# Performance work log

Hardware: AMD Instinct MI355X
Metric: run time of the kernel (lower is better)

## Reference

```python
import jax, jax.numpy as jnp
import numpy as np

D_MODEL = 1024
N_HEADS = 16
HEAD_DIM = D_MODEL // N_HEADS
ALPHA = 1.5
SEQ, BATCH = 4096, 8


def reduced_sparsemax(z, alpha):
    # projection of z/alpha onto the simplex along the last axis
    zs = z / alpha
    z_sorted = -jnp.sort(-zs, axis=-1)          # descending sort
    z_cumsum = jnp.cumsum(z_sorted, axis=-1)
    d = zs.shape[-1]
    r = jnp.arange(1, d + 1, dtype=zs.dtype)
    support = (z_sorted - (z_cumsum - 1.0) / r) > 0
    k = jnp.sum(support, axis=-1, keepdims=True)
    k_safe = jnp.clip(k, 1, None)
    tau_sum = jnp.take_along_axis(z_cumsum, k_safe - 1, axis=-1)
    tau = (tau_sum - 1.0) / k_safe.astype(zs.dtype)
    return jnp.clip(zs - tau, 0.0, None)


def setup_inputs() -> dict:
    key = jax.random.key(0)
    ks = jax.random.split(key, 11)
    s = 0.02
    return {
        "query": jax.random.normal(ks[0], (SEQ, BATCH, D_MODEL), jnp.float32),
        "key":   jax.random.normal(ks[1], (SEQ, BATCH, D_MODEL), jnp.float32),
        "value": jax.random.normal(ks[2], (SEQ, BATCH, D_MODEL), jnp.float32),
        "Wq": jax.random.normal(ks[3], (D_MODEL, D_MODEL), jnp.float32) * s,
        "bq": jnp.zeros((D_MODEL,), jnp.float32),
        "Wk": jax.random.normal(ks[4], (D_MODEL, D_MODEL), jnp.float32) * s,
        "bk": jnp.zeros((D_MODEL,), jnp.float32),
        "Wv": jax.random.normal(ks[5], (D_MODEL, D_MODEL), jnp.float32) * s,
        "bv": jnp.zeros((D_MODEL,), jnp.float32),
        "Wo": jax.random.normal(ks[6], (D_MODEL, D_MODEL), jnp.float32) * s,
        "bo": jnp.zeros((D_MODEL,), jnp.float32),
    }


def reference(query, key, value, Wq, bq, Wk, bk, Wv, bv, Wo, bo):
    A, B, D = query.shape  # (seq, batch, d_model) per the torch code's indexing
    H, hd = N_HEADS, HEAD_DIM
    Q = query @ Wq.T + bq
    K = key @ Wk.T + bk
    V = value @ Wv.T + bv
    # view(A, B, H, hd).transpose(0, 1) -> (B, A, H, hd)
    Q = jnp.swapaxes(Q.reshape(A, B, H, hd), 0, 1)
    K = jnp.swapaxes(K.reshape(A, B, H, hd), 0, 1)
    V = jnp.swapaxes(V.reshape(A, B, H, hd), 0, 1)
    # NOTE: faithful to the original code, attention is across HEADS:
    # scores shape (B, A, H, H)
    scores = jnp.einsum('bahd,bagd->bahg', Q, K) / jnp.sqrt(
        jnp.asarray(hd, jnp.float32))
    attn = reduced_sparsemax(scores, ALPHA)
    attn_out = jnp.einsum('bahg,bagd->bahd', attn, V)  # (B, A, H, hd)
    # transpose(1,2).view(B, -1, D): (B, H, A, hd) flattened to (B, A, D)
    attn_out = jnp.swapaxes(attn_out, 1, 2).reshape(B, -1, D)
    out = attn_out @ Wo.T + bo           # (B, A, D)
    return jnp.swapaxes(out, 0, 1)       # (A, B, D)
```

## Files before the change

### kernel.cpp

```cpp
#include <hip/hip_runtime.h>
#include <hip/hip_bf16.h>
#include <stdint.h>

typedef __bf16 bf16_t;
typedef __bf16 bf16x4 __attribute__((ext_vector_type(4)));
typedef __bf16 bf16x8 __attribute__((ext_vector_type(8)));
typedef float  f32x4  __attribute__((ext_vector_type(4)));

#define AS_G __attribute__((address_space(1)))
#define AS_L __attribute__((address_space(3)))

__global__ void cast_f32_bf16(const float* __restrict__ src, bf16_t* __restrict__ dst) {
    int i = blockIdx.x * 256 + threadIdx.x;
    float4 v = ((const float4*)src)[i];
    bf16x4 o;
    o.x = (bf16_t)v.x; o.y = (bf16_t)v.y; o.z = (bf16_t)v.z; o.w = (bf16_t)v.w;
    ((bf16x4*)dst)[i] = o;
}

template<int OUT_BF16>
__global__ void gemm_bt_kernel(const bf16_t* __restrict__ A,
                               const bf16_t* __restrict__ Bt,
                               const float* __restrict__ bias,
                               void* __restrict__ Cout,
                               int M, int N, int K) {
    __shared__ bf16_t As[128 * 32];
    __shared__ bf16_t Bs[128 * 32];
    const int tid  = threadIdx.x;
    const int wave = tid >> 6, lane = tid & 63;
    const int quad = lane >> 4, r16 = lane & 15;
    const int wm = (wave >> 1) * 64, wn = (wave & 1) * 64;
    const int m0 = blockIdx.y * 128, n0 = blockIdx.x * 128;

    const int sr = (wave << 5) + (lane >> 2);
    const int ce = (lane & 3) << 3;
    const bf16_t* ga = A  + (size_t)(m0 + sr) * K + ce;
    const bf16_t* gb = Bt + (size_t)(n0 + sr) * K + ce;
    bf16_t* la = &As[sr * 32 + ce];
    bf16_t* lb = &Bs[sr * 32 + ce];

    f32x4 acc[4][4] = {};

    for (int k0 = 0; k0 < K; k0 += 32) {
        __builtin_amdgcn_global_load_lds((AS_G void*)(ga + k0),              (AS_L void*)la,             16, 0, 0);
        __builtin_amdgcn_global_load_lds((AS_G void*)(ga + k0 + 16 * (size_t)K), (AS_L void*)(la + 16 * 32), 16, 0, 0);
        __builtin_amdgcn_global_load_lds((AS_G void*)(gb + k0),              (AS_L void*)lb,             16, 0, 0);
        __builtin_amdgcn_global_load_lds((AS_G void*)(gb + k0 + 16 * (size_t)K), (AS_L void*)(lb + 16 * 32), 16, 0, 0);
        __syncthreads();

        bf16x8 aF[4], bF[4];
#pragma unroll
        for (int t = 0; t < 4; ++t) {
            aF[t] = *(const bf16x8*)&As[(wm + t * 16 + r16) * 32 + quad * 8];
            bF[t] = *(const bf16x8*)&Bs[(wn + t * 16 + r16) * 32 + quad * 8];
        }
#pragma unroll
        for (int tm = 0; tm < 4; ++tm)
#pragma unroll
            for (int tn = 0; tn < 4; ++tn)
                acc[tm][tn] = __builtin_amdgcn_mfma_f32_16x16x32_bf16(aF[tm], bF[tn], acc[tm][tn], 0, 0, 0);
        __syncthreads();
    }

    float bv[4];
#pragma unroll
    for (int tn = 0; tn < 4; ++tn) bv[tn] = bias[n0 + wn + tn * 16 + r16];

#pragma unroll
    for (int tm = 0; tm < 4; ++tm) {
#pragma unroll
        for (int r = 0; r < 4; ++r) {
            const int m = m0 + wm + tm * 16 + quad * 4 + r;
#pragma unroll
            for (int tn = 0; tn < 4; ++tn) {
                const int n = n0 + wn + tn * 16 + r16;
                const float v = acc[tm][tn][r] + bv[tn];
                if (OUT_BF16) ((bf16_t*)Cout)[(size_t)m * N + n] = (bf16_t)v;
                else          ((float*)Cout)[(size_t)m * N + n]  = v;
            }
        }
    }
}

__global__ void attn_kernel(const bf16_t* __restrict__ Q, const bf16_t* __restrict__ K,
                            const bf16_t* __restrict__ V, bf16_t* __restrict__ M2) {
    __shared__ float zs_s[4][16][17];
    __shared__ float tau_s[4][16];
    const int wave = threadIdx.x >> 6, lane = threadIdx.x & 63;
    const int quad = lane >> 4, g16 = lane & 15;
    const int p = blockIdx.x * 4 + wave;
    const int a = p >> 3, b = p & 7;
    const bf16_t* q = Q + (size_t)p * 1024;
    const bf16_t* k = K + (size_t)p * 1024;
    const bf16_t* v = V + (size_t)p * 1024;

    bf16x8 qa0 = *(const bf16x8*)(q + g16 * 64 + quad * 8);
    bf16x8 qa1 = *(const bf16x8*)(q + g16 * 64 + 32 + quad * 8);
    bf16x8 ka0 = *(const bf16x8*)(k + g16 * 64 + quad * 8);
    bf16x8 ka1 = *(const bf16x8*)(k + g16 * 64 + 32 + quad * 8);
    f32x4 sc = {0.f, 0.f, 0.f, 0.f};
    sc = __builtin_amdgcn_mfma_f32_16x16x32_bf16(qa0, ka0, sc, 0, 0, 0);
    sc = __builtin_amdgcn_mfma_f32_16x16x32_bf16(qa1, ka1, sc, 0, 0, 0);

    const float inv = 1.0f / 12.0f;
#pragma unroll
    for (int r = 0; r < 4; ++r) zs_s[wave][quad * 4 + r][g16] = sc[r] * inv;
    __syncthreads();

    if (lane < 16) {
        float z[16];
#pragma unroll
        for (int j = 0; j < 16; ++j) z[j] = zs_s[wave][lane][j];
#pragma unroll
        for (int kk = 2; kk <= 16; kk <<= 1) {
#pragma unroll
            for (int j = kk >> 1; j > 0; j >>= 1) {
#pragma unroll
                for (int i = 0; i < 16; ++i) {
                    int ixj = i ^ j;
                    if (ixj > i) {
                        bool desc = ((i & kk) == 0);
                        float zi = z[i], zj = z[ixj];
                        bool sw = desc ? (zi < zj) : (zi > zj);
                        z[i]   = sw ? zj : zi;
                        z[ixj] = sw ? zi : zj;
                    }
                }
            }
        }
        float cum = 0.f, csel = 0.f;
        int ksel = 1;
#pragma unroll
        for (int j = 0; j < 16; ++j) {
            cum += z[j];
            bool sup = z[j] * (float)(j + 1) > (cum - 1.0f);
            ksel = sup ? (j + 1) : ksel;
            csel = sup ? cum : csel;
        }
        tau_s[wave][lane] = (csel - 1.0f) / (float)ksel;
    }
    __syncthreads();

#pragma unroll
    for (int r = 0; r < 4; ++r) {
        float av = sc[r] * inv - tau_s[wave][quad * 4 + r];
        zs_s[wave][quad * 4 + r][g16] = av > 0.f ? av : 0.f;
    }
    __syncthreads();

    bf16x8 aP;
#pragma unroll
    for (int j = 0; j < 8; ++j) {
        float f = (quad < 2) ? zs_s[wave][g16][quad * 8 + j] : 0.f;
        aP[j] = (bf16_t)f;
    }
#pragma unroll
    for (int c = 0; c < 4; ++c) {
        bf16x8 bV;
#pragma unroll
        for (int j = 0; j < 8; ++j) {
            int g = quad * 8 + j;
            bV[j] = (quad < 2) ? v[g * 64 + c * 16 + g16] : (bf16_t)0.f;
        }
        f32x4 oc = {0.f, 0.f, 0.f, 0.f};
        oc = __builtin_amdgcn_mfma_f32_16x16x32_bf16(aP, bV, oc, 0, 0, 0);
#pragma unroll
        for (int r = 0; r < 4; ++r) {
            int h = quad * 4 + r;
            int e = c * 16 + g16;
            int rr = (h << 8) + (a >> 4);
            int c2 = ((a & 15) << 6) + e;
            M2[((size_t)(rr * 8 + b)) * 1024 + c2] = (bf16_t)oc[r];
        }
    }
}

extern "C" void kernel_launch(void* const* d_in, const int* in_sizes, int n_in,
                              void* d_out, int out_size, void* d_ws, size_t ws_size,
                              hipStream_t stream) {
    (void)in_sizes; (void)n_in; (void)out_size; (void)ws_size;
    const float* query = (const float*)d_in[0];
    const float* key   = (const float*)d_in[1];
    const float* value = (const float*)d_in[2];
    const float* Wq = (const float*)d_in[3];
    const float* bq = (const float*)d_in[4];
    const float* Wk = (const float*)d_in[5];
    const float* bk = (const float*)d_in[6];
    const float* Wv = (const float*)d_in[7];
    const float* bv = (const float*)d_in[8];
    const float* Wo = (const float*)d_in[9];
    const float* bo = (const float*)d_in[10];

    const int M = 32768, D = 1024;
    const size_t MD = (size_t)M * D;

    uint8_t* ws = (uint8_t*)d_ws;
    bf16_t* abuf = (bf16_t*)ws;
    bf16_t* Qb   = (bf16_t*)(ws + MD * 2);
    bf16_t* Kb   = Qb + MD;
    bf16_t* Vb   = Kb + MD;
    bf16_t* M2   = Vb + MD;
    bf16_t* Wqb  = M2 + MD;
    bf16_t* Wkb  = Wqb + (size_t)D * D;
    bf16_t* Wvb  = Wkb + (size_t)D * D;
    bf16_t* Wob  = Wvb + (size_t)D * D;

    const int wBlocks = D * D / 1024;
    const int aBlocks = (int)(MD / 1024);
    cast_f32_bf16<<<wBlocks, 256, 0, stream>>>(Wq, Wqb);
    cast_f32_bf16<<<wBlocks, 256, 0, stream>>>(Wk, Wkb);
    cast_f32_bf16<<<wBlocks, 256, 0, stream>>>(Wv, Wvb);
    cast_f32_bf16<<<wBlocks, 256, 0, stream>>>(Wo, Wob);

    dim3 gg(D / 128, M / 128);

    cast_f32_bf16<<<aBlocks, 256, 0, stream>>>(query, abuf);
    gemm_bt_kernel<1><<<gg, 256, 0, stream>>>(abuf, Wqb, bq, Qb, M, D, D);
    cast_f32_bf16<<<aBlocks, 256, 0, stream>>>(key, abuf);
    gemm_bt_kernel<1><<<gg, 256, 0, stream>>>(abuf, Wkb, bk, Kb, M, D, D);
    cast_f32_bf16<<<aBlocks, 256, 0, stream>>>(value, abuf);
    gemm_bt_kernel<1><<<gg, 256, 0, stream>>>(abuf, Wvb, bv, Vb, M, D, D);

    attn_kernel<<<M / 4, 256, 0, stream>>>(Qb, Kb, Vb, M2);

    gemm_bt_kernel<0><<<gg, 256, 0, stream>>>(M2, Wob, bo, (float*)d_out, M, D, D);
}
```

Baseline: 875.2 us.

## Rework GEMM into 256x256 tiles with 4-stage LDS pipeline and swizzling

The GEMM kernel moves from 128x128 tiles with 4 waves to 256x256 tiles with 8 waves, using a 4-deep ring of LDS buffers. Global-to-LDS loads are issued three K-steps ahead and gated by vmcnt waits, which removes the per-step double barrier. LDS columns are XOR-swizzled to avoid bank conflicts, the block index is remapped for cache locality, and setprio raises priority during MFMA bursts. The aim is to hide memory latency and raise MFMA utilisation across all four projection GEMMs. The cost is 128KB of LDS per block and high register pressure from 32 accumulators per lane, which may limit occupancy.

```diff
diff --git a/kernel.cpp b/kernel.cpp
--- a/kernel.cpp
+++ b/kernel.cpp
@@ -19,61 +19,87 @@
 }
 
 template<int OUT_BF16>
-__global__ void gemm_bt_kernel(const bf16_t* __restrict__ A,
-                               const bf16_t* __restrict__ Bt,
-                               const float* __restrict__ bias,
-                               void* __restrict__ Cout,
-                               int M, int N, int K) {
-    __shared__ bf16_t As[128 * 32];
-    __shared__ bf16_t Bs[128 * 32];
+__global__ __launch_bounds__(512, 2)
+void gemm_bt_kernel(const bf16_t* __restrict__ A,
+                    const bf16_t* __restrict__ Bt,
+                    const float* __restrict__ bias,
+                    void* __restrict__ Cout,
+                    int M, int N, int K) {
+    __shared__ bf16_t smem[4][2][256 * 32];
+
     const int tid  = threadIdx.x;
     const int wave = tid >> 6, lane = tid & 63;
     const int quad = lane >> 4, r16 = lane & 15;
-    const int wm = (wave >> 1) * 64, wn = (wave & 1) * 64;
-    const int m0 = blockIdx.y * 128, n0 = blockIdx.x * 128;
-
-    const int sr = (wave << 5) + (lane >> 2);
-    const int ce = (lane & 3) << 3;
-    const bf16_t* ga = A  + (size_t)(m0 + sr) * K + ce;
-    const bf16_t* gb = Bt + (size_t)(n0 + sr) * K + ce;
-    bf16_t* la = &As[sr * 32 + ce];
-    bf16_t* lb = &Bs[sr * 32 + ce];
-
-    f32x4 acc[4][4] = {};
-
-    for (int k0 = 0; k0 < K; k0 += 32) {
-        __builtin_amdgcn_global_load_lds((AS_G void*)(ga + k0),              (AS_L void*)la,             16, 0, 0);
-        __builtin_amdgcn_global_load_lds((AS_G void*)(ga + k0 + 16 * (size_t)K), (AS_L void*)(la + 16 * 32), 16, 0, 0);
-        __builtin_amdgcn_global_load_lds((AS_G void*)(gb + k0),              (AS_L void*)lb,             16, 0, 0);
-        __builtin_amdgcn_global_load_lds((AS_G void*)(gb + k0 + 16 * (size_t)K), (AS_L void*)(lb + 16 * 32), 16, 0, 0);
-        __syncthreads();
-
-        bf16x8 aF[4], bF[4];
-#pragma unroll
-        for (int t = 0; t < 4; ++t) {
-            aF[t] = *(const bf16x8*)&As[(wm + t * 16 + r16) * 32 + quad * 8];
-            bF[t] = *(const bf16x8*)&Bs[(wn + t * 16 + r16) * 32 + quad * 8];
-        }
-#pragma unroll
-        for (int tm = 0; tm < 4; ++tm)
+    const int wr = wave >> 2, wc = wave & 3;
+
+    const int nbx = N >> 8;
+    const int cpx = gridDim.x >> 3;
+    const int swz = (blockIdx.x & 7) * cpx + (blockIdx.x >> 3);
+    const int m0 = (swz / nbx) << 8;
+    const int n0 = (swz % nbx) << 8;
+
+    const int c0 = tid, c1 = 512 + tid;
+    const int r0 = c0 >> 2, cc0 = c0 & 3;
+    const int r1 = c1 >> 2, cc1 = c1 & 3;
+    const int s0 = (r0 & 3) ^ ((r0 >> 2) & 3);
+    const int s1 = (r1 & 3) ^ ((r1 >> 2) & 3);
+    const bf16_t* gA0 = A  + (size_t)(m0 + r0) * K + ((cc0 ^ s0) << 3);
+    const bf16_t* gA1 = A  + (size_t)(m0 + r1) * K + ((cc1 ^ s1) << 3);
+    const bf16_t* gB0 = Bt + (size_t)(n0 + r0) * K + ((cc0 ^ s0) << 3);
+    const bf16_t* gB1 = Bt + (size_t)(n0 + r1) * K + ((cc1 ^ s1) << 3);
+
+#define STAGE(bufi, kt) do {                                                                    \
+        const int _ko = (kt) << 5;                                                              \
+        __builtin_amdgcn_global_load_lds((AS_G void*)(gA0 + _ko), (AS_L void*)(&smem[bufi][0][c0 * 8]), 16, 0, 0); \
+        __builtin_amdgcn_global_load_lds((AS_G void*)(gA1 + _ko), (AS_L void*)(&smem[bufi][0][c1 * 8]), 16, 0, 0); \
+        __builtin_amdgcn_global_load_lds((AS_G void*)(gB0 + _ko), (AS_L void*)(&smem[bufi][1][c0 * 8]), 16, 0, 0); \
+        __builtin_amdgcn_global_load_lds((AS_G void*)(gB1 + _ko), (AS_L void*)(&smem[bufi][1][c1 * 8]), 16, 0, 0); \
+    } while (0)
+
+    f32x4 acc[8][4] = {};
+    const int NT = K >> 5;
+
+    STAGE(0, 0); STAGE(1, 1); STAGE(2, 2);
+
+    const int swzc = quad ^ (r16 & 3) ^ ((r16 >> 2) & 3);
+    const int aoff = ((wr * 128 + r16) << 5) + (swzc << 3);
+    const int boff = ((wc * 64  + r16) << 5) + (swzc << 3);
+
+    for (int t = 0; t < NT; ++t) {
+        asm volatile("s_waitcnt vmcnt(8)\n\ts_barrier" ::: "memory");
+
+        if (t + 3 < NT) STAGE((t + 3) & 3, t + 3);
+
+        const bf16_t* pA = &smem[t & 3][0][0];
+        const bf16_t* pB = &smem[t & 3][1][0];
+        bf16x8 aF[8], bF[4];
+#pragma unroll
+        for (int i = 0; i < 8; ++i) aF[i] = *(const bf16x8*)(pA + aoff + i * 512);
+#pragma unroll
+        for (int i = 0; i < 4; ++i) bF[i] = *(const bf16x8*)(pB + boff + i * 512);
+
+        __builtin_amdgcn_s_setprio(1);
+#pragma unroll
+        for (int tm = 0; tm < 8; ++tm)
 #pragma unroll
             for (int tn = 0; tn < 4; ++tn)
                 acc[tm][tn] = __builtin_amdgcn_mfma_f32_16x16x32_bf16(aF[tm], bF[tn], acc[tm][tn], 0, 0, 0);
-        __syncthreads();
-    }
+        __builtin_amdgcn_s_setprio(0);
+    }
+#undef STAGE
 
     float bv[4];
 #pragma unroll
-    for (int tn = 0; tn < 4; ++tn) bv[tn] = bias[n0 + wn + tn * 16 + r16];
-
-#pragma unroll
-    for (int tm = 0; tm < 4; ++tm) {
+    for (int tn = 0; tn < 4; ++tn) bv[tn] = bias[n0 + wc * 64 + tn * 16 + r16];
+
+#pragma unroll
+    for (int tm = 0; tm < 8; ++tm) {
 #pragma unroll
         for (int r = 0; r < 4; ++r) {
-            const int m = m0 + wm + tm * 16 + quad * 4 + r;
+            const int m = m0 + wr * 128 + tm * 16 + quad * 4 + r;
 #pragma unroll
             for (int tn = 0; tn < 4; ++tn) {
-                const int n = n0 + wn + tn * 16 + r16;
+                const int n = n0 + wc * 64 + tn * 16 + r16;
                 const float v = acc[tm][tn][r] + bv[tn];
                 if (OUT_BF16) ((bf16_t*)Cout)[(size_t)m * N + n] = (bf16_t)v;
                 else          ((float*)Cout)[(size_t)m * N + n]  = v;
@@ -212,16 +238,16 @@
     cast_f32_bf16<<<wBlocks, 256, 0, stream>>>(Wv, Wvb);
     cast_f32_bf16<<<wBlocks, 256, 0, stream>>>(Wo, Wob);
 
-    dim3 gg(D / 128, M / 128);
+    const int gblk = (M / 256) * (D / 256);
 
     cast_f32_bf16<<<aBlocks, 256, 0, stream>>>(query, abuf);
-    gemm_bt_kernel<1><<<gg, 256, 0, stream>>>(abuf, Wqb, bq, Qb, M, D, D);
+    gemm_bt_kernel<1><<<gblk, 512, 0, stream>>>(abuf, Wqb, bq, Qb, M, D, D);
     cast_f32_bf16<<<aBlocks, 256, 0, stream>>>(key, abuf);
-    gemm_bt_kernel<1><<<gg, 256, 0, stream>>>(abuf, Wkb, bk, Kb, M, D, D);
+    gemm_bt_kernel<1><<<gblk, 512, 0, stream>>>(abuf, Wkb, bk, Kb, M, D, D);
     cast_f32_bf16<<<aBlocks, 256, 0, stream>>>(value, abuf);
-    gemm_bt_kernel<1><<<gg, 256, 0, stream>>>(abuf, Wvb, bv, Vb, M, D, D);
+    gemm_bt_kernel<1><<<gblk, 512, 0, stream>>>(abuf, Wvb, bv, Vb, M, D, D);
 
     attn_kernel<<<M / 4, 256, 0, stream>>>(Qb, Kb, Vb, M2);
 
-    gemm_bt_kernel<0><<<gg, 256, 0, stream>>>(M2, Wob, bo, (float*)d_out, M, D, D);
-}
+    gemm_bt_kernel<0><<<gblk, 512, 0, stream>>>(M2, Wob, bo, (float*)d_out, M, D, D);
+}
```

Result: faster. 795.6 us (-9.1%).
